# Kernel optimization log

Measured on AMD Instinct MI355X. Metric: run time of the kernel, lower is better.

## Reference

```python
import jax, jax.numpy as jnp
import numpy as np
from jax import lax

IN_DIM = 512
MID = IN_DIM // 2          # 256
HEADS = 8
B, H, W = 16, 64, 64
BN_EPS = 1e-5
NORM_EPS = 1e-12


def setup_inputs() -> dict:
    key = jax.random.key(0)
    ks = jax.random.split(key, 16)
    r = lambda k, shape, s=0.02: jax.random.normal(k, shape, dtype=jnp.float32) * s
    return {
        "x": jax.random.normal(ks[0], (B, IN_DIM, H, W), dtype=jnp.float32),
        "reduce_w": r(ks[1], (MID, IN_DIM)),
        "reduce_b": jnp.zeros((MID,), jnp.float32),
        "dw_w": r(ks[2], (MID, 1, 3, 3), 0.1),
        "dw_b": jnp.zeros((MID,), jnp.float32),
        "bn_gamma": jnp.ones((MID,), jnp.float32),
        "bn_beta": jnp.zeros((MID,), jnp.float32),
        "bn_mean": r(ks[3], (MID,), 0.1),
        "bn_var": jnp.ones((MID,), jnp.float32),
        "gate_w1": r(ks[4], (MID // 8, MID)),
        "gate_b1": jnp.zeros((MID // 8,), jnp.float32),
        "gate_w2": r(ks[5], (MID, MID // 8)),
        "gate_b2": jnp.zeros((MID,), jnp.float32),
        "temperature": jnp.ones((HEADS, 1, 1), jnp.float32),
        "post_w": r(ks[6], (IN_DIM, 2 * MID)),
        "post_b": jnp.zeros((IN_DIM,), jnp.float32),
    }


def reference(x, reduce_w, reduce_b, dw_w, dw_b, bn_gamma, bn_beta, bn_mean, bn_var,
              gate_w1, gate_b1, gate_w2, gate_b2, temperature, post_w, post_b):
    Bsz, C, Hh, Ww = x.shape
    # reduce (1x1 conv) -> depthwise 3x3 -> BN (eval stats) -> ReLU
    xr = jnp.einsum('bchw,oc->bohw', x, reduce_w) + reduce_b[:, None, None]
    xr = lax.conv_general_dilated(xr, dw_w, (1, 1), 'SAME',
                                  feature_group_count=MID,
                                  dimension_numbers=('NCHW', 'OIHW', 'NCHW'))
    xr = xr + dw_b[:, None, None]
    inv = bn_gamma / jnp.sqrt(bn_var + BN_EPS)
    xr = (xr - bn_mean[:, None, None]) * inv[:, None, None] + bn_beta[:, None, None]
    xr = jax.nn.relu(xr)

    # FFT channel attention
    fft_feat = jnp.fft.fft2(xr, norm='ortho')              # complex64 [B,MID,H,W]
    HWn = Hh * Ww
    qkv = fft_feat.reshape(Bsz, HEADS, MID // HEADS, HWn)  # b h c n (complex)
    nrm = jnp.sqrt(jnp.sum(jnp.abs(qkv) ** 2, axis=-1, keepdims=True))
    qn = qkv / jnp.maximum(nrm, NORM_EPS)                  # L2-normalize complex rows
    attn = jnp.einsum('bhcn,bhdn->bhcd', qn, qn)           # complex, no conjugate (matches torch)
    attn = attn * temperature                               # [h,1,1] real broadcast
    attn = jax.nn.softmax(attn.real, axis=-1)
    out = jnp.einsum('bhcd,bhdn->bhcn', attn, qkv.real)
    out = out.reshape(Bsz, MID, Hh, Ww).astype(jnp.complex64)
    out = jnp.fft.ifft2(out, norm='ortho').real

    # SE gate + frequency-domain recombine (default fft norm, as in torch)
    g = jnp.mean(xr, axis=(-2, -1))                         # [B,MID]
    g = jax.nn.relu(g @ gate_w1.T + gate_b1)
    g = jax.nn.sigmoid(g @ gate_w2.T + gate_b2)
    gated = g[:, :, None, None] * xr
    fwm = jnp.fft.ifft2(fft_feat * jnp.fft.fft2(gated)).real

    fused = jnp.concatenate([out, fwm], axis=1)             # [B,2*MID,H,W]
    y = jnp.einsum('bchw,oc->bohw', fused, post_w) + post_b[:, None, None] + x
    return y
```

## Files before the change

kernel.cpp:

```cpp
#include <hip/hip_runtime.h>
#include <math.h>

#define BATCH 16
#define CIN   512
#define MID   256
#define HW    4096
#define HEADS 8
#define CH    32
#define KSPL  8
#define PI2   6.2831853071795864769f
#define RT2H  0.70710678118654752440f

typedef __attribute__((ext_vector_type(8))) short short8;
typedef __attribute__((ext_vector_type(4))) float floatx4;
typedef __attribute__((ext_vector_type(16))) float floatx16;

__device__ inline unsigned short f2b(float f) {
  union { float f; unsigned int u; } v; v.f = f;
  unsigned int u = v.u;
  unsigned int r = (u + 0x7fffu + ((u >> 16) & 1u)) >> 16;
  return (unsigned short)r;
}

__device__ __forceinline__ int swidx(int r, int n) {
  return (r << 6) + (n ^ (r & 15));
}

__device__ __forceinline__ void cmadd(float2& a, const float2 x,
                                      const float wr, const float wi) {
  a.x = fmaf(x.x, wr, a.x); a.x = fmaf(-x.y, wi, a.x);
  a.y = fmaf(x.x, wi, a.y); a.y = fmaf(x.y, wr, a.y);
}

template<int SGN, int AXIS>
__device__ __forceinline__ void dft64_pass(float2* __restrict__ buf,
                                           const float2* __restrict__ tw,
                                           const int tid)
{
  constexpr float W8R[8] = {1.f, RT2H, 0.f, -RT2H, -1.f, -RT2H, 0.f, RT2H};
  constexpr float W8I[8] = {0.f, RT2H, 1.f, RT2H, 0.f, -RT2H, -1.f, -RT2H};
  const int line = tid & 63;
  const int wv = tid >> 6;
  float2 xa[2][8];

  #pragma unroll
  for (int t = 0; t < 2; ++t) {
    const int b = wv + (t << 2);
    #pragma unroll
    for (int a = 0; a < 8; ++a) {
      const int i = (a << 3) + b;
      xa[t][a] = buf[AXIS ? swidx(line, i) : swidx(i, line)];
    }
  }
  __syncthreads();
  #pragma unroll
  for (int t = 0; t < 2; ++t) {
    const int b = wv + (t << 2);
    #pragma unroll
    for (int d = 0; d < 8; ++d) {
      float2 y = make_float2(0.f, 0.f);
      #pragma unroll
      for (int a = 0; a < 8; ++a) {
        const int j = (a * d) & 7;
        cmadd(y, xa[t][a], W8R[j], (float)SGN * W8I[j]);
      }
      const float2 tb = tw[(b * d) & 63];
      float2 z;
      z.x = y.x * tb.x - y.y * tb.y;
      z.y = y.x * tb.y + y.y * tb.x;
      const int i = (b << 3) + d;
      buf[AXIS ? swidx(line, i) : swidx(i, line)] = z;
    }
  }
  __syncthreads();

  #pragma unroll
  for (int t = 0; t < 2; ++t) {
    const int d = wv + (t << 2);
    #pragma unroll
    for (int b = 0; b < 8; ++b) {
      const int i = (b << 3) + d;
      xa[t][b] = buf[AXIS ? swidx(line, i) : swidx(i, line)];
    }
  }
  __syncthreads();
  #pragma unroll
  for (int t = 0; t < 2; ++t) {
    const int d = wv + (t << 2);
    #pragma unroll
    for (int c = 0; c < 8; ++c) {
      float2 s = make_float2(0.f, 0.f);
      #pragma unroll
      for (int b = 0; b < 8; ++b) {
        const int j = (b * c) & 7;
        cmadd(s, xa[t][b], W8R[j], (float)SGN * W8I[j]);
      }
      const int i = (c << 3) + d;
      buf[AXIS ? swidx(line, i) : swidx(i, line)] = s;
    }
  }
  __syncthreads();
}

__global__ __launch_bounds__(256) void k_castw(
    const float* __restrict__ rw, const float* __restrict__ pw,
    unsigned short* __restrict__ rwB, unsigned short* __restrict__ pwB)
{
  int i = blockIdx.x * 256 + threadIdx.x;
  if (i < MID * CIN) rwB[i] = f2b(rw[i]);
  if (i < CIN * 2 * MID) pwB[i] = f2b(pw[i]);
}


__global__ __launch_bounds__(256) void k_gemm_red(
    const unsigned short* __restrict__ A, const float* __restrict__ Bg0,
    const float* __restrict__ bias, float* __restrict__ out)
{
  __shared__ __align__(16) char As[128 * 144];
  __shared__ __align__(16) char Bs[128 * 144];
  const int tid = threadIdx.x;
  const int n0 = blockIdx.x << 7;
  const int m0 = blockIdx.y << 7;
  const int b  = blockIdx.z;
  const int lane = tid & 63, wave = tid >> 6;
  const int wm = (wave >> 1) << 6, wn = (wave & 1) << 6;
  const int l16 = lane & 15, quad = lane >> 4;
  const float* Bg = Bg0 + (size_t)b * CIN * HW;
  floatx4 acc[4][4] = {};
  for (int k0 = 0; k0 < CIN; k0 += 64) {
    #pragma unroll
    for (int it = 0; it < 4; ++it) {
      int l = tid + (it << 8);
      int m = l >> 3, ko = (l & 7) << 3;
      *(uint4*)(As + m * 144 + (ko << 1)) =
          *(const uint4*)&A[(size_t)(m0 + m) * CIN + k0 + ko];
    }
    #pragma unroll
    for (int it = 0; it < 2; ++it) {
      int id = tid + (it << 8);
      int np = id & 63, q = id >> 6;
      const float* r0 = Bg + (size_t)(k0 + (q << 3)) * HW + n0 + (np << 1);
      unsigned int d0[4], d1[4];
      #pragma unroll
      for (int p = 0; p < 4; ++p) {
        float2 va = *(const float2*)(r0 + (size_t)(2 * p) * HW);
        float2 vb = *(const float2*)(r0 + (size_t)(2 * p + 1) * HW);
        d0[p] = (unsigned int)f2b(va.x) | ((unsigned int)f2b(vb.x) << 16);
        d1[p] = (unsigned int)f2b(va.y) | ((unsigned int)f2b(vb.y) << 16);
      }
      char* dst = Bs + (np << 1) * 144 + ((q ^ (np & 7)) << 4);
      *(uint4*)dst = make_uint4(d0[0], d0[1], d0[2], d0[3]);
      *(uint4*)(dst + 144) = make_uint4(d1[0], d1[1], d1[2], d1[3]);
    }
    __syncthreads();
    #pragma unroll
    for (int kk = 0; kk < 2; ++kk) {
      short8 af[4], bf[4];
      #pragma unroll
      for (int mi = 0; mi < 4; ++mi)
        af[mi] = *(const short8*)(As + (wm + (mi << 4) + l16) * 144 + (kk << 6) + (quad << 4));
      #pragma unroll
      for (int ni = 0; ni < 4; ++ni) {
        int n = wn + (ni << 4) + l16;
        bf[ni] = *(const short8*)(Bs + n * 144 + ((((kk << 2) + quad) ^ ((n >> 1) & 7)) << 4));
      }
      #pragma unroll
      for (int mi = 0; mi < 4; ++mi)
        #pragma unroll
        for (int ni = 0; ni < 4; ++ni)
          acc[mi][ni] = __builtin_amdgcn_mfma_f32_16x16x32_bf16(af[mi], bf[ni], acc[mi][ni], 0, 0, 0);
    }
    __syncthreads();
  }
  #pragma unroll
  for (int mi = 0; mi < 4; ++mi)
    #pragma unroll
    for (int reg = 0; reg < 4; ++reg) {
      int m = m0 + wm + (mi << 4) + (quad << 2) + reg;
      float bv = bias[m];
      size_t base = ((size_t)b * MID + m) * HW + n0 + wn + l16;
      #pragma unroll
      for (int ni = 0; ni < 4; ++ni)
        out[base + (ni << 4)] = acc[mi][ni][reg] + bv;
    }
}

__global__ __launch_bounds__(256) void k_gemm_post(
    const unsigned short* __restrict__ A, const float* __restrict__ fftf,
    const float* __restrict__ bias, const float* __restrict__ x,
    float* __restrict__ y)
{
  __shared__ __align__(16) char As[128 * 144];
  __shared__ __align__(16) char Bs[128 * 144];
  const int tid = threadIdx.x;
  const int n0 = blockIdx.x << 7;
  const int m0 = blockIdx.y << 7;
  const int b  = blockIdx.z;
  const int lane = tid & 63, wave = tid >> 6;
  const int wm = (wave >> 1) << 6, wn = (wave & 1) << 6;
  const int l16 = lane & 15, quad = lane >> 4;
  floatx4 acc[4][4] = {};
  for (int k0 = 0; k0 < 2 * MID; k0 += 64) {
    #pragma unroll
    for (int it = 0; it < 4; ++it) {
      int l = tid + (it << 8);
      int m = l >> 3, ko = (l & 7) << 3;
      *(uint4*)(As + m * 144 + (ko << 1)) =
          *(const uint4*)&A[(size_t)(m0 + m) * (2 * MID) + k0 + ko];
    }
    #pragma unroll
    for (int it = 0; it < 2; ++it) {
      int id = tid + (it << 8);
      int np = id & 63, q = id >> 6;
      int c0 = k0 + (q << 3);
      const unsigned short* bp = (const unsigned short*)
          (fftf + (size_t)(b * MID + (c0 & 255)) * (2 * HW) + ((c0 < MID) ? HW : 0));
      const unsigned int* bp32 = (const unsigned int*)(bp + n0) + np;
      unsigned int d0[4], d1[4];
      #pragma unroll
      for (int p = 0; p < 4; ++p) {
        unsigned int a  = bp32[(size_t)(2 * p) * (2 * HW)];
        unsigned int bq = bp32[(size_t)(2 * p + 1) * (2 * HW)];
        d0[p] = (a & 0xffffu) | (bq << 16);
        d1[p] = (a >> 16) | (bq & 0xffff0000u);
      }
      char* dst = Bs + (np << 1) * 144 + ((q ^ (np & 7)) << 4);
      *(uint4*)dst = make_uint4(d0[0], d0[1], d0[2], d0[3]);
      *(uint4*)(dst + 144) = make_uint4(d1[0], d1[1], d1[2], d1[3]);
    }
    __syncthreads();
    #pragma unroll
    for (int kk = 0; kk < 2; ++kk) {
      short8 af[4], bf[4];
      #pragma unroll
      for (int mi = 0; mi < 4; ++mi)
        af[mi] = *(const short8*)(As + (wm + (mi << 4) + l16) * 144 + (kk << 6) + (quad << 4));
      #pragma unroll
      for (int ni = 0; ni < 4; ++ni) {
        int n = wn + (ni << 4) + l16;
        bf[ni] = *(const short8*)(Bs + n * 144 + ((((kk << 2) + quad) ^ ((n >> 1) & 7)) << 4));
      }
      #pragma unroll
      for (int mi = 0; mi < 4; ++mi)
        #pragma unroll
        for (int ni = 0; ni < 4; ++ni)
          acc[mi][ni] = __builtin_amdgcn_mfma_f32_16x16x32_bf16(af[mi], bf[ni], acc[mi][ni], 0, 0, 0);
    }
    __syncthreads();
  }
  #pragma unroll
  for (int mi = 0; mi < 4; ++mi)
    #pragma unroll
    for (int reg = 0; reg < 4; ++reg) {
      int m = m0 + wm + (mi << 4) + (quad << 2) + reg;
      float bv = bias[m];
      size_t base = ((size_t)b * CIN + m) * HW + n0 + wn + l16;
      #pragma unroll
      for (int ni = 0; ni < 4; ++ni)
        y[base + (ni << 4)] = acc[mi][ni][reg] + bv + x[base + (ni << 4)];
    }
}

__global__ __launch_bounds__(256) void k_dwbn(
    const float* __restrict__ in, const float* __restrict__ dww,
    const float* __restrict__ dwb, const float* __restrict__ gamma,
    const float* __restrict__ beta, const float* __restrict__ mean,
    const float* __restrict__ var, float* __restrict__ out,
    float* __restrict__ g0)
{
  __shared__ float pl[HW];
  __shared__ float red[256];
  const int p = blockIdx.x;
  const int c = p & (MID - 1);
  const int tid = threadIdx.x;
  const float* ip = in + (size_t)p * HW;
  for (int l = tid; l < HW; l += 256) pl[l] = ip[l];
  float wreg[9];
  #pragma unroll
  for (int i = 0; i < 9; ++i) wreg[i] = dww[c * 9 + i];
  const float bconv = dwb[c];
  const float inv = gamma[c] * rsqrtf(var[c] + 1e-5f);
  const float mu = mean[c], bt = beta[c];
  __syncthreads();
  float lsum = 0.f;
  float* op = out + (size_t)p * HW;
  for (int l = tid; l < HW; l += 256) {
    int y = l >> 6, xx0 = l & 63;
    float s = bconv;
    #pragma unroll
    for (int ky = 0; ky < 3; ++ky) {
      int yy = y + ky - 1;
      if (yy < 0 || yy >= 64) continue;
      #pragma unroll
      for (int kx = 0; kx < 3; ++kx) {
        int xx = xx0 + kx - 1;
        if (xx < 0 || xx >= 64) continue;
        s = fmaf(pl[(yy << 6) + xx], wreg[ky * 3 + kx], s);
      }
    }
    s = (s - mu) * inv + bt;
    s = fmaxf(s, 0.f);
    op[l] = s;
    lsum += s;
  }
  red[tid] = lsum;
  __syncthreads();
  for (int st = 128; st > 0; st >>= 1) {
    if (tid < st) red[tid] += red[tid + st];
    __syncthreads();
  }
  if (tid == 0) g0[p] = red[0] * (1.f / HW);
}

__global__ __launch_bounds__(256) void k_gate(
    const float* __restrict__ g0, const float* __restrict__ w1,
    const float* __restrict__ b1, const float* __restrict__ w2,
    const float* __restrict__ b2, float* __restrict__ g)
{
  __shared__ float gs[MID];
  __shared__ float hs[32];
  const int b = blockIdx.x;
  const int tid = threadIdx.x;
  gs[tid] = g0[b * MID + tid];
  __syncthreads();
  if (tid < 32) {
    float s = b1[tid];
    for (int c = 0; c < MID; ++c) s = fmaf(gs[c], w1[tid * MID + c], s);
    hs[tid] = fmaxf(s, 0.f);
  }
  __syncthreads();
  float s = b2[tid];
  #pragma unroll
  for (int j = 0; j < 32; ++j) s = fmaf(hs[j], w2[tid * 32 + j], s);
  g[b * MID + tid] = 1.f / (1.f + expf(-s));
}

__global__ __launch_bounds__(256) void k_fft_fwd(
    const float* __restrict__ in, float* __restrict__ outf,
    float* __restrict__ Nbuf)
{
  __shared__ float2 buf[64 * 64];
  __shared__ float2 tw[64];
  __shared__ float red[256];
  const int tid = threadIdx.x;
  const int p = blockIdx.x;
  if (tid < 64) {
    float ang = -PI2 * (float)tid * (1.f / 64.f);
    tw[tid] = make_float2(cosf(ang), sinf(ang));
  }
  const float* ip = in + (size_t)p * HW;
  for (int l = tid; l < HW; l += 256)
    buf[swidx(l >> 6, l & 63)] = make_float2(ip[l], 0.f);
  __syncthreads();
  dft64_pass<-1, 0>(buf, tw, tid);
  dft64_pass<-1, 1>(buf, tw, tid);
  float2* op = (float2*)(outf + (size_t)p * (2 * HW));
  float lsum = 0.f;
  for (int l = tid; l < HW; l += 256) {
    float2 v = buf[swidx(l >> 6, l & 63)];
    float vx = v.x * (1.f / 64.f), vy = v.y * (1.f / 64.f);
    op[l] = make_float2(vx, vy);
    lsum = fmaf(vx, vx, fmaf(vy, vy, lsum));
  }
  red[tid] = lsum;
  __syncthreads();
  for (int st = 128; st > 0; st >>= 1) {
    if (tid < st) red[tid] += red[tid + st];
    __syncthreads();
  }
  if (tid == 0) Nbuf[p] = red[0];
}

__global__ __launch_bounds__(256) void k_attn_s(
    const float* __restrict__ fftf, float* __restrict__ Sbuf)
{
  __shared__ float red[4 * 1024];
  const int bh = blockIdx.y;
  const int ks = blockIdx.x;
  const int b = bh >> 3, h = bh & 7;
  const int tid = threadIdx.x;
  const int lane = tid & 63, wave = tid >> 6;
  const int r  = lane & 31;
  const int hi = lane >> 5;
  const float* rowp = fftf + (size_t)(b * MID + h * CH + r) * (2 * HW)
                    + (size_t)ks * (2 * HW / KSPL) + wave * (2 * HW / KSPL / 4)
                    + (hi << 3);
  floatx16 acc = {};
  #pragma unroll
  for (int st = 0; st < (2 * HW / KSPL / 4) / 16; ++st) {
    float4 f0 = *(const float4*)(rowp + st * 16);
    float4 f1 = *(const float4*)(rowp + st * 16 + 4);
    short8 a;
    a[0] = (short)f2b(f0.x); a[1] = (short)f2b(f0.y);
    a[2] = (short)f2b(f0.z); a[3] = (short)f2b(f0.w);
    a[4] = (short)f2b(f1.x); a[5] = (short)f2b(f1.y);
    a[6] = (short)f2b(f1.z); a[7] = (short)f2b(f1.w);
    uint4 av = *(uint4*)&a;
    uint4 bv = make_uint4(av.x ^ 0x80000000u, av.y ^ 0x80000000u,
                          av.z ^ 0x80000000u, av.w ^ 0x80000000u);
    short8 bn = *(short8*)&bv;
    acc = __builtin_amdgcn_mfma_f32_32x32x16_bf16(a, bn, acc, 0, 0, 0);
  }
  #pragma unroll
  for (int i = 0; i < 16; ++i) {
    const int row = (i & 3) + ((i >> 2) << 3) + (hi << 2);
    red[wave * 1024 + row * 32 + r] = acc[i];
  }
  __syncthreads();
  float* Sp = Sbuf + ((size_t)bh * KSPL + ks) * 1024;
  #pragma unroll
  for (int e = tid; e < 1024; e += 256)
    Sp[e] = red[e] + red[1024 + e] + red[2048 + e] + red[3072 + e];
}

__global__ __launch_bounds__(64) void k_attn_sm(
    const float* __restrict__ Sbuf, const float* __restrict__ Nbuf,
    const float* __restrict__ temp, float* __restrict__ Pbuf)
{
  const int bh = blockIdx.x;
  const int h = bh & 7;
  const int tid = threadIdx.x;
  if (tid < 32) {
    float nc = fmaxf(sqrtf(Nbuf[bh * 32 + tid]), 1e-12f);
    float tmp = temp[h];
    const float* Sp = Sbuf + (size_t)bh * (KSPL * 1024) + tid * 32;
    float vals[32];
    float vmax = -1e30f;
    #pragma unroll
    for (int d = 0; d < 32; ++d) {
      float s = 0.f;
      #pragma unroll
      for (int ksx = 0; ksx < KSPL; ++ksx) s += Sp[ksx * 1024 + d];
      float nd = fmaxf(sqrtf(Nbuf[bh * 32 + d]), 1e-12f);
      float v = s / (nc * nd) * tmp;
      vals[d] = v;
      vmax = fmaxf(vmax, v);
    }
    float sum = 0.f;
    #pragma unroll
    for (int d = 0; d < 32; ++d) {
      float e = expf(vals[d] - vmax);
      vals[d] = e;
      sum += e;
    }
    float rinv = 1.f / sum;
    float* Pp = Pbuf + (size_t)bh * 1024 + tid * 32;
    #pragma unroll
    for (int d = 0; d < 32; ++d) Pp[d] = vals[d] * rinv;
  }
}

__global__ __launch_bounds__(256) void k_attn_o(
    const float* __restrict__ fftf, const float* __restrict__ Pbuf,
    float* __restrict__ outw)
{
  const int bh = blockIdx.y;
  const int n0 = blockIdx.x << 9;
  const int b = bh >> 3, h = bh & 7;
  const float2* Q = (const float2*)fftf + ((size_t)b * MID + (size_t)h * CH) * HW;
  __shared__ float P[1024];
  __shared__ float Lr[32 * 514];
  const int tid = threadIdx.x;
  for (int l = tid; l < 1024; l += 256) P[l] = Pbuf[(size_t)bh * 1024 + l];
  for (int l = tid; l < 32 * 512; l += 256) {
    int r = l >> 9, nn = l & 511;
    Lr[r * 514 + nn] = Q[(size_t)r * HW + n0 + nn].x;
  }
  __syncthreads();
  const float2* Lr2 = (const float2*)Lr;
  const float4* P4 = (const float4*)P;
  float* orow = outw + ((size_t)b * MID + (size_t)h * CH) * HW + n0;
  #pragma unroll 4
  for (int c = 0; c < 32; ++c) {
    float s0 = 0.f, s1 = 0.f;
    #pragma unroll
    for (int j = 0; j < 8; ++j) {
      float4 pv = P4[c * 8 + j];
      int d = j << 2;
      float2 v0 = Lr2[(d + 0) * 257 + tid];
      float2 v1 = Lr2[(d + 1) * 257 + tid];
      float2 v2 = Lr2[(d + 2) * 257 + tid];
      float2 v3 = Lr2[(d + 3) * 257 + tid];
      s0 = fmaf(pv.x, v0.x, s0); s1 = fmaf(pv.x, v0.y, s1);
      s0 = fmaf(pv.y, v1.x, s0); s1 = fmaf(pv.y, v1.y, s1);
      s0 = fmaf(pv.z, v2.x, s0); s1 = fmaf(pv.z, v2.y, s1);
      s0 = fmaf(pv.w, v3.x, s0); s1 = fmaf(pv.w, v3.y, s1);
    }
    ((float2*)(orow + (size_t)c * HW))[tid] = make_float2(s0, s1);
  }
}

__global__ __launch_bounds__(256) void k_ifft_re(
    const float* __restrict__ in, float* __restrict__ fftf)
{
  __shared__ float2 buf[64 * 64];
  __shared__ float2 tw[64];
  const int tid = threadIdx.x;
  const int p = blockIdx.x;
  if (tid < 64) {
    float ang = -PI2 * (float)tid * (1.f / 64.f);
    tw[tid] = make_float2(cosf(ang), sinf(ang));
  }
  const float* ip = in + (size_t)p * HW;
  for (int l = tid; l < HW; l += 256)
    buf[swidx(l >> 6, l & 63)] = make_float2(ip[l], 0.f);
  __syncthreads();
  dft64_pass<-1, 0>(buf, tw, tid);
  dft64_pass<-1, 1>(buf, tw, tid);
  unsigned short* op = (unsigned short*)(fftf + (size_t)p * (2 * HW) + HW);
  for (int l = tid; l < HW; l += 256) {
    float2 v = buf[swidx(l >> 6, l & 63)];
    op[l] = f2b(v.x * (1.f / 64.f));
  }
}

__global__ __launch_bounds__(256) void k_fwm(
    float* __restrict__ fftf, const float* __restrict__ g)
{
  __shared__ float2 buf[64 * 64];
  __shared__ float2 tw[64];
  const int tid = threadIdx.x;
  const int p = blockIdx.x;
  if (tid < 64) {
    float ang = PI2 * (float)tid * (1.f / 64.f);
    tw[tid] = make_float2(cosf(ang), sinf(ang));
  }
  float* plane = fftf + (size_t)p * (2 * HW);
  const float2* F = (const float2*)plane;
  for (int l = tid; l < HW; l += 256) {
    float2 v = F[l];
    buf[swidx(l >> 6, l & 63)] = make_float2(v.x * v.x - v.y * v.y, 2.f * v.x * v.y);
  }
  __syncthreads();
  dft64_pass<1, 0>(buf, tw, tid);
  dft64_pass<1, 1>(buf, tw, tid);
  const float gg = g[p] * (1.f / 64.f);
  unsigned short* ob = (unsigned short*)plane;
  for (int l = tid; l < HW; l += 256) {
    float2 v = buf[swidx(l >> 6, l & 63)];
    ob[l] = f2b(v.x * gg);
  }
}

extern "C" void kernel_launch(void* const* d_in, const int* in_sizes, int n_in,
                              void* d_out, int out_size, void* d_ws, size_t ws_size,
                              hipStream_t stream)
{
  const float* x    = (const float*)d_in[0];
  const float* rw   = (const float*)d_in[1];
  const float* rb   = (const float*)d_in[2];
  const float* dww  = (const float*)d_in[3];
  const float* dwb  = (const float*)d_in[4];
  const float* bng  = (const float*)d_in[5];
  const float* bnb  = (const float*)d_in[6];
  const float* bnm  = (const float*)d_in[7];
  const float* bnv  = (const float*)d_in[8];
  const float* gw1  = (const float*)d_in[9];
  const float* gb1  = (const float*)d_in[10];
  const float* gw2  = (const float*)d_in[11];
  const float* gb2  = (const float*)d_in[12];
  const float* temp = (const float*)d_in[13];
  const float* pw   = (const float*)d_in[14];
  const float* pb   = (const float*)d_in[15];
  float* y = (float*)d_out;

  float* ws = (float*)d_ws;
  const size_t PL = (size_t)BATCH * MID * HW;
  float* xr   = ws;
  float* fftf = ws + PL;
  float* g0   = ws + 3 * PL;
  float* gg   = g0 + BATCH * MID;
  float* Nbuf = gg + BATCH * MID;
  unsigned short* rwB = (unsigned short*)(Nbuf + BATCH * MID);
  unsigned short* pwB = rwB + MID * CIN;
  float* Sbuf = xr;
  float* Pbuf = xr + (size_t)BATCH * HEADS * KSPL * 1024;
  float* xr0  = y;

  k_castw    <<<dim3(1024),            256, 0, stream>>>(rw, pw, rwB, pwB);
  k_gemm_red <<<dim3(32, 2, BATCH),    256, 0, stream>>>(rwB, x, rb, xr0);
  k_dwbn     <<<dim3(BATCH * MID),     256, 0, stream>>>(xr0, dww, dwb, bng, bnb, bnm, bnv, xr, g0);
  k_gate     <<<dim3(BATCH),           256, 0, stream>>>(g0, gw1, gb1, gw2, gb2, gg);
  k_fft_fwd  <<<dim3(BATCH * MID),     256, 0, stream>>>(xr, fftf, Nbuf);
  k_attn_s   <<<dim3(KSPL, BATCH * HEADS), 256, 0, stream>>>(fftf, Sbuf);
  k_attn_sm  <<<dim3(BATCH * HEADS),   64,  0, stream>>>(Sbuf, Nbuf, temp, Pbuf);
  k_attn_o   <<<dim3(8, BATCH * HEADS), 256, 0, stream>>>(fftf, Pbuf, xr0);
  k_fwm      <<<dim3(BATCH * MID),     256, 0, stream>>>(fftf, gg);
  k_ifft_re  <<<dim3(BATCH * MID),     256, 0, stream>>>(xr0, fftf);
  k_gemm_post<<<dim3(32, 4, BATCH),    256, 0, stream>>>(pwB, fftf, pb, x, y);
}
```

Before: 655.9 us.

## Double-buffer B tiles with register prefetch and read A fragments from global

Both bf16 GEMM kernels (reduce and post) now keep two LDS buffers for the B tile. The next K-slice is prefetched into registers while the MFMAs run on the current buffer, then converted and stored into the other buffer, so only one barrier is needed per iteration. The A (weight) tile is no longer staged in shared memory; each wave loads its MFMA fragments straight from global memory, relying on cache reuse. The aim is to hide global load latency and cut LDS traffic and barriers, at the cost of more registers and uncoalesced, repeated global reads of A across waves.

Result: slower. 779.2 us (+18.8%).

```diff
diff --git a/kernel.cpp b/kernel.cpp
--- a/kernel.cpp
+++ b/kernel.cpp
@@ -116,8 +116,7 @@
     const unsigned short* __restrict__ A, const float* __restrict__ Bg0,
     const float* __restrict__ bias, float* __restrict__ out)
 {
-  __shared__ __align__(16) char As[128 * 144];
-  __shared__ __align__(16) char Bs[128 * 144];
+  __shared__ __align__(16) char Bs[2][128 * 144];
   const int tid = threadIdx.x;
   const int n0 = blockIdx.x << 7;
   const int m0 = blockIdx.y << 7;
@@ -125,44 +124,62 @@
   const int lane = tid & 63, wave = tid >> 6;
   const int wm = (wave >> 1) << 6, wn = (wave & 1) << 6;
   const int l16 = lane & 15, quad = lane >> 4;
+  const int np = tid & 63;
+  const int qw = tid >> 6;
   const float* Bg = Bg0 + (size_t)b * CIN * HW;
   floatx4 acc[4][4] = {};
-  for (int k0 = 0; k0 < CIN; k0 += 64) {
-    #pragma unroll
-    for (int it = 0; it < 4; ++it) {
-      int l = tid + (it << 8);
-      int m = l >> 3, ko = (l & 7) << 3;
-      *(uint4*)(As + m * 144 + (ko << 1)) =
-          *(const uint4*)&A[(size_t)(m0 + m) * CIN + k0 + ko];
-    }
-    #pragma unroll
-    for (int it = 0; it < 2; ++it) {
-      int id = tid + (it << 8);
-      int np = id & 63, q = id >> 6;
-      const float* r0 = Bg + (size_t)(k0 + (q << 3)) * HW + n0 + (np << 1);
-      unsigned int d0[4], d1[4];
-      #pragma unroll
-      for (int p = 0; p < 4; ++p) {
-        float2 va = *(const float2*)(r0 + (size_t)(2 * p) * HW);
-        float2 vb = *(const float2*)(r0 + (size_t)(2 * p + 1) * HW);
-        d0[p] = (unsigned int)f2b(va.x) | ((unsigned int)f2b(vb.x) << 16);
-        d1[p] = (unsigned int)f2b(va.y) | ((unsigned int)f2b(vb.y) << 16);
-      }
-      char* dst = Bs + (np << 1) * 144 + ((q ^ (np & 7)) << 4);
-      *(uint4*)dst = make_uint4(d0[0], d0[1], d0[2], d0[3]);
-      *(uint4*)(dst + 144) = make_uint4(d1[0], d1[1], d1[2], d1[3]);
-    }
+  float2 pva[2][4], pvb[2][4];
+
+  #pragma unroll
+  for (int it = 0; it < 2; ++it) {
+    int q = qw + (it << 2);
+    const float* r0 = Bg + (size_t)(q << 3) * HW + n0 + (np << 1);
+    #pragma unroll
+    for (int p = 0; p < 4; ++p) {
+      pva[it][p] = *(const float2*)(r0 + (size_t)(2 * p) * HW);
+      pvb[it][p] = *(const float2*)(r0 + (size_t)(2 * p + 1) * HW);
+    }
+  }
+  #pragma unroll
+  for (int it = 0; it < 2; ++it) {
+    int q = qw + (it << 2);
+    unsigned int d0[4], d1[4];
+    #pragma unroll
+    for (int p = 0; p < 4; ++p) {
+      d0[p] = (unsigned)f2b(pva[it][p].x) | ((unsigned)f2b(pvb[it][p].x) << 16);
+      d1[p] = (unsigned)f2b(pva[it][p].y) | ((unsigned)f2b(pvb[it][p].y) << 16);
+    }
+    char* dst = Bs[0] + (np << 1) * 144 + ((q ^ (np & 7)) << 4);
+    *(uint4*)dst = make_uint4(d0[0], d0[1], d0[2], d0[3]);
+    *(uint4*)(dst + 144) = make_uint4(d1[0], d1[1], d1[2], d1[3]);
+  }
+  int cur = 0;
+  for (int t = 0; t < 8; ++t) {
+    const int k0 = t << 6;
     __syncthreads();
+    if (t < 7) {
+      #pragma unroll
+      for (int it = 0; it < 2; ++it) {
+        int q = qw + (it << 2);
+        const float* r0 = Bg + (size_t)(k0 + 64 + (q << 3)) * HW + n0 + (np << 1);
+        #pragma unroll
+        for (int p = 0; p < 4; ++p) {
+          pva[it][p] = *(const float2*)(r0 + (size_t)(2 * p) * HW);
+          pvb[it][p] = *(const float2*)(r0 + (size_t)(2 * p + 1) * HW);
+        }
+      }
+    }
     #pragma unroll
     for (int kk = 0; kk < 2; ++kk) {
       short8 af[4], bf[4];
       #pragma unroll
       for (int mi = 0; mi < 4; ++mi)
-        af[mi] = *(const short8*)(As + (wm + (mi << 4) + l16) * 144 + (kk << 6) + (quad << 4));
+        af[mi] = *(const short8*)&A[(size_t)(m0 + wm + (mi << 4) + l16) * CIN
+                                    + k0 + (kk << 5) + (quad << 3)];
       #pragma unroll
       for (int ni = 0; ni < 4; ++ni) {
         int n = wn + (ni << 4) + l16;
-        bf[ni] = *(const short8*)(Bs + n * 144 + ((((kk << 2) + quad) ^ ((n >> 1) & 7)) << 4));
+        bf[ni] = *(const short8*)(Bs[cur] + n * 144 + ((((kk << 2) + quad) ^ ((n >> 1) & 7)) << 4));
       }
       #pragma unroll
       for (int mi = 0; mi < 4; ++mi)
@@ -170,7 +187,22 @@
         for (int ni = 0; ni < 4; ++ni)
           acc[mi][ni] = __builtin_amdgcn_mfma_f32_16x16x32_bf16(af[mi], bf[ni], acc[mi][ni], 0, 0, 0);
     }
-    __syncthreads();
+    if (t < 7) {
+      #pragma unroll
+      for (int it = 0; it < 2; ++it) {
+        int q = qw + (it << 2);
+        unsigned int d0[4], d1[4];
+        #pragma unroll
+        for (int p = 0; p < 4; ++p) {
+          d0[p] = (unsigned)f2b(pva[it][p].x) | ((unsigned)f2b(pvb[it][p].x) << 16);
+          d1[p] = (unsigned)f2b(pva[it][p].y) | ((unsigned)f2b(pvb[it][p].y) << 16);
+        }
+        char* dst = Bs[cur ^ 1] + (np << 1) * 144 + ((q ^ (np & 7)) << 4);
+        *(uint4*)dst = make_uint4(d0[0], d0[1], d0[2], d0[3]);
+        *(uint4*)(dst + 144) = make_uint4(d1[0], d1[1], d1[2], d1[3]);
+      }
+    }
+    cur ^= 1;
   }
   #pragma unroll
   for (int mi = 0; mi < 4; ++mi)
@@ -190,8 +222,7 @@
     const float* __restrict__ bias, const float* __restrict__ x,
     float* __restrict__ y)
 {
-  __shared__ __align__(16) char As[128 * 144];
-  __shared__ __align__(16) char Bs[128 * 144];
+  __shared__ __align__(16) char Bs[2][128 * 144];
   const int tid = threadIdx.x;
   const int n0 = blockIdx.x << 7;
   const int m0 = blockIdx.y << 7;
@@ -199,46 +230,67 @@
   const int lane = tid & 63, wave = tid >> 6;
   const int wm = (wave >> 1) << 6, wn = (wave & 1) << 6;
   const int l16 = lane & 15, quad = lane >> 4;
+  const int np = tid & 63;
+  const int qw = tid >> 6;
   floatx4 acc[4][4] = {};
-  for (int k0 = 0; k0 < 2 * MID; k0 += 64) {
-    #pragma unroll
-    for (int it = 0; it < 4; ++it) {
-      int l = tid + (it << 8);
-      int m = l >> 3, ko = (l & 7) << 3;
-      *(uint4*)(As + m * 144 + (ko << 1)) =
-          *(const uint4*)&A[(size_t)(m0 + m) * (2 * MID) + k0 + ko];
-    }
-    #pragma unroll
-    for (int it = 0; it < 2; ++it) {
-      int id = tid + (it << 8);
-      int np = id & 63, q = id >> 6;
-      int c0 = k0 + (q << 3);
-      const unsigned short* bp = (const unsigned short*)
-          (fftf + (size_t)(b * MID + (c0 & 255)) * (2 * HW) + ((c0 < MID) ? HW : 0));
-      const unsigned int* bp32 = (const unsigned int*)(bp + n0) + np;
-      unsigned int d0[4], d1[4];
-      #pragma unroll
-      for (int p = 0; p < 4; ++p) {
-        unsigned int a  = bp32[(size_t)(2 * p) * (2 * HW)];
-        unsigned int bq = bp32[(size_t)(2 * p + 1) * (2 * HW)];
-        d0[p] = (a & 0xffffu) | (bq << 16);
-        d1[p] = (a >> 16) | (bq & 0xffff0000u);
-      }
-      char* dst = Bs + (np << 1) * 144 + ((q ^ (np & 7)) << 4);
-      *(uint4*)dst = make_uint4(d0[0], d0[1], d0[2], d0[3]);
-      *(uint4*)(dst + 144) = make_uint4(d1[0], d1[1], d1[2], d1[3]);
-    }
+  unsigned int ua[2][4], ub[2][4];
+
+  #pragma unroll
+  for (int it = 0; it < 2; ++it) {
+    int q = qw + (it << 2);
+    int c0 = q << 3;
+    const unsigned short* bp = (const unsigned short*)
+        (fftf + (size_t)(b * MID + (c0 & 255)) * (2 * HW) + ((c0 < MID) ? HW : 0));
+    const unsigned int* bp32 = (const unsigned int*)(bp + n0) + np;
+    #pragma unroll
+    for (int p = 0; p < 4; ++p) {
+      ua[it][p] = bp32[(size_t)(2 * p) * (2 * HW)];
+      ub[it][p] = bp32[(size_t)(2 * p + 1) * (2 * HW)];
+    }
+  }
+  #pragma unroll
+  for (int it = 0; it < 2; ++it) {
+    int q = qw + (it << 2);
+    unsigned int d0[4], d1[4];
+    #pragma unroll
+    for (int p = 0; p < 4; ++p) {
+      d0[p] = (ua[it][p] & 0xffffu) | (ub[it][p] << 16);
+      d1[p] = (ua[it][p] >> 16) | (ub[it][p] & 0xffff0000u);
+    }
+    char* dst = Bs[0] + (np << 1) * 144 + ((q ^ (np & 7)) << 4);
+    *(uint4*)dst = make_uint4(d0[0], d0[1], d0[2], d0[3]);
+    *(uint4*)(dst + 144) = make_uint4(d1[0], d1[1], d1[2], d1[3]);
+  }
+  int cur = 0;
+  for (int t = 0; t < 8; ++t) {
+    const int k0 = t << 6;
     __syncthreads();
+    if (t < 7) {
+      #pragma unroll
+      for (int it = 0; it < 2; ++it) {
+        int q = qw + (it << 2);
+        int c0 = k0 + 64 + (q << 3);
+        const unsigned short* bp = (const unsigned short*)
+            (fftf + (size_t)(b * MID + (c0 & 255)) * (2 * HW) + ((c0 < MID) ? HW : 0));
+        const unsigned int* bp32 = (const unsigned int*)(bp + n0) + np;
+        #pragma unroll
+        for (int p = 0; p < 4; ++p) {
+          ua[it][p] = bp32[(size_t)(2 * p) * (2 * HW)];
+          ub[it][p] = bp32[(size_t)(2 * p + 1) * (2 * HW)];
+        }
+      }
+    }
     #pragma unroll
     for (int kk = 0; kk < 2; ++kk) {
       short8 af[4], bf[4];
       #pragma unroll
       for (int mi = 0; mi < 4; ++mi)
-        af[mi] = *(const short8*)(As + (wm + (mi << 4) + l16) * 144 + (kk << 6) + (quad << 4));
+        af[mi] = *(const short8*)&A[(size_t)(m0 + wm + (mi << 4) + l16) * (2 * MID)
+                                    + k0 + (kk << 5) + (quad << 3)];
       #pragma unroll
       for (int ni = 0; ni < 4; ++ni) {
         int n = wn + (ni << 4) + l16;
-        bf[ni] = *(const short8*)(Bs + n * 144 + ((((kk << 2) + quad) ^ ((n >> 1) & 7)) << 4));
+        bf[ni] = *(const short8*)(Bs[cur] + n * 144 + ((((kk << 2) + quad) ^ ((n >> 1) & 7)) << 4));
       }
       #pragma unroll
       for (int mi = 0; mi < 4; ++mi)
@@ -246,7 +298,22 @@
         for (int ni = 0; ni < 4; ++ni)
           acc[mi][ni] = __builtin_amdgcn_mfma_f32_16x16x32_bf16(af[mi], bf[ni], acc[mi][ni], 0, 0, 0);
     }
-    __syncthreads();
+    if (t < 7) {
+      #pragma unroll
+      for (int it = 0; it < 2; ++it) {
+        int q = qw + (it << 2);
+        unsigned int d0[4], d1[4];
+        #pragma unroll
+        for (int p = 0; p < 4; ++p) {
+          d0[p] = (ua[it][p] & 0xffffu) | (ub[it][p] << 16);
+          d1[p] = (ua[it][p] >> 16) | (ub[it][p] & 0xffff0000u);
+        }
+        char* dst = Bs[cur ^ 1] + (np << 1) * 144 + ((q ^ (np & 7)) << 4);
+        *(uint4*)dst = make_uint4(d0[0], d0[1], d0[2], d0[3]);
+        *(uint4*)(dst + 144) = make_uint4(d1[0], d1[1], d1[2], d1[3]);
+      }
+    }
+    cur ^= 1;
   }
   #pragma unroll
   for (int mi = 0; mi < 4; ++mi)
```
